# Optimization experiments

Measured on AMD Instinct MI355X. Metric: run time of the kernel, lower is better.

## Reference

```python
import jax, jax.numpy as jnp
import numpy as np

D_MODEL = 1024
D_STATE = 16
EXPANSION = 2
GROUPS = 16
D_INNER = EXPANSION * D_MODEL          # 2048
GROUP_SIZE = D_INNER // GROUPS         # 128
B, T = 2, 1024


def _rmsnorm(x, g, eps=1e-6):
    return x * jax.lax.rsqrt(jnp.mean(x * x, axis=-1, keepdims=True) + eps) * g


def setup_inputs() -> dict:
    key = jax.random.key(0)
    ks = jax.random.split(key, 8)
    s_in = 1.0 / np.sqrt(D_MODEL)
    s_inner = 1.0 / np.sqrt(D_INNER)
    s_ff = 1.0 / np.sqrt(4 * D_MODEL)
    return {
        "x": jax.random.normal(ks[0], (B, T, D_MODEL), dtype=jnp.float32),
        "A_log": jnp.log(jnp.linspace(1.0, float(D_STATE), D_STATE)).astype(jnp.float32),
        "g1": jnp.ones((D_MODEL,), jnp.float32),
        "g2": jnp.ones((D_MODEL,), jnp.float32),
        "W_in": jax.random.normal(ks[1], (2 * D_INNER, D_MODEL), jnp.float32) * s_in,
        "W_param": jax.random.normal(ks[2], (GROUPS * (1 + 2 * D_STATE), D_INNER), jnp.float32) * s_inner,
        "W_out": jax.random.normal(ks[3], (D_MODEL, D_INNER), jnp.float32) * s_inner,
        "W_ffn1": jax.random.normal(ks[4], (4 * D_MODEL, D_MODEL), jnp.float32) * s_in,
        "b_ffn1": jnp.zeros((4 * D_MODEL,), jnp.float32),
        "W_ffn2": jax.random.normal(ks[5], (D_MODEL, 4 * D_MODEL), jnp.float32) * s_ff,
        "b_ffn2": jnp.zeros((D_MODEL,), jnp.float32),
    }


def _ssm(u, delta, b, c, A_log):
    # u,delta: [B,T,D]; b,c: [B,T,D,N]. Sequential recurrence equivalent to
    # the module's chunked cumprod/cumsum formulation.
    A = -jnp.exp(A_log)                                   # [N]
    deltaA = jnp.clip(delta[..., None] * A, -10.0, 10.0)  # [B,T,D,N]
    expA = jnp.exp(deltaA)
    frac_exact = (expA - 1.0) / (A + 1e-12)
    frac = jnp.where(jnp.abs(deltaA) < 1e-4, delta[..., None], frac_exact)
    Bu = frac * (b * u[..., None])                        # [B,T,D,N]

    def step(h, inp):
        Ah_t, Bu_t, c_t = inp                             # [B,D,N] each
        h = Ah_t * h + Bu_t
        return h, jnp.sum(h * c_t, axis=-1)               # y_t: [B,D]

    tm = lambda a: jnp.moveaxis(a, 1, 0)                  # time-major [T,B,D,N]
    h0 = jnp.zeros(u.shape[:1] + u.shape[2:] + (A.shape[0],), u.dtype)
    _, ys = jax.lax.scan(step, h0, (tm(expA), tm(Bu), tm(c)))
    return jnp.moveaxis(ys, 0, 1)                         # [B,T,D]


def reference(x, A_log, g1, g2, W_in, W_param, W_out, W_ffn1, b_ffn1, W_ffn2, b_ffn2):
    Bsz, Tlen, _ = x.shape
    z = _rmsnorm(x, g1)
    xz_gate = jnp.einsum('btd,ed->bte', z, W_in)          # [B,T,2*D_inner]
    xz, gate = jnp.split(xz_gate, 2, axis=-1)
    xz = jax.nn.silu(xz)

    params = jnp.einsum('btd,pd->btp', xz, W_param)
    params = params.reshape(Bsz, Tlen, GROUPS, 1 + 2 * D_STATE)
    delta_g = params[..., :1]                             # [B,T,G,1]
    b_g = params[..., 1:1 + D_STATE]                      # [B,T,G,N]
    c_g = params[..., 1 + D_STATE:]                       # [B,T,G,N]
    delta = jax.nn.softplus(jnp.repeat(delta_g[..., 0], GROUP_SIZE, axis=2))  # [B,T,D_inner]
    b = jnp.repeat(b_g, GROUP_SIZE, axis=2)               # [B,T,D_inner,N]
    c = jnp.repeat(c_g, GROUP_SIZE, axis=2)

    y_ssm = _ssm(xz, delta, b, c, A_log)                  # [B,T,D_inner]
    y = y_ssm * jax.nn.silu(gate)
    y = jnp.einsum('bte,de->btd', y, W_out)
    x = x + y                                             # residual (dropout/droppath = identity in eval)

    h2 = _rmsnorm(x, g2)
    ffn = jnp.einsum('btf,df->btd',
                     jax.nn.silu(jnp.einsum('btd,fd->btf', h2, W_ffn1) + b_ffn1),
                     W_ffn2) + b_ffn2
    return x + ffn
```

## Files before the change

### kernel.cpp

```cpp
#include <hip/hip_runtime.h>
#include <hip/hip_bf16.h>
#include <stdint.h>

#define ROWS 2048
#define DM   1024
#define DI   2048
#define PPAD 640

typedef __bf16 bf16_t;
typedef __attribute__((ext_vector_type(8))) __bf16 bf16x8;
typedef __attribute__((ext_vector_type(4))) __bf16 bf16x4;
typedef __attribute__((ext_vector_type(4))) float f32x4;
typedef __attribute__((address_space(1))) void gvoid_t;
typedef __attribute__((address_space(3))) void lvoid_t;

__global__ __launch_bounds__(256) void prep0(const float* __restrict__ W_in,
                                             const float* __restrict__ W_param,
                                             bf16_t* o_in, bf16_t* o_par,
                                             const float* __restrict__ x,
                                             const float* __restrict__ g1,
                                             bf16_t* __restrict__ zb) {
  int tid = threadIdx.x;
  if (blockIdx.x >= 5376) {
    int row = blockIdx.x - 5376;
    const float4 v = *(const float4*)(x + (int64_t)row * DM + tid * 4);
    float ss = v.x * v.x + v.y * v.y + v.z * v.z + v.w * v.w;
#pragma unroll
    for (int o = 32; o; o >>= 1) ss += __shfl_xor(ss, o, 64);
    __shared__ float red[4];
    if ((tid & 63) == 0) red[tid >> 6] = ss;
    __syncthreads();
    float tot = red[0] + red[1] + red[2] + red[3];
    float sc = rsqrtf(tot * (1.0f / DM) + 1e-6f);
    const float4 gv = *(const float4*)(g1 + tid * 4);
    bf16_t* o = zb + (int64_t)row * DM + tid * 4;
    o[0] = (bf16_t)(v.x * sc * gv.x);
    o[1] = (bf16_t)(v.y * sc * gv.y);
    o[2] = (bf16_t)(v.z * sc * gv.z);
    o[3] = (bf16_t)(v.w * sc * gv.w);
    return;
  }
  if (blockIdx.x >= 4096) {
    int64_t e = (((int64_t)(blockIdx.x - 4096)) * 256 + tid) * 4;
    int row = (int)(e >> 11), col = (int)(e & 2047);
    float4 v = make_float4(0.f, 0.f, 0.f, 0.f);
    if (row < 528) v = *(const float4*)(W_param + (int64_t)row * 2048 + col);
    bf16_t* o = o_par + e;
    o[0] = (bf16_t)v.x; o[1] = (bf16_t)v.y; o[2] = (bf16_t)v.z; o[3] = (bf16_t)v.w;
    return;
  }
  int64_t e = ((int64_t)blockIdx.x * 256 + tid) * 4;
  float4 v = *(const float4*)(W_in + e);
  bf16_t* o = o_in + e;
  o[0] = (bf16_t)v.x; o[1] = (bf16_t)v.y; o[2] = (bf16_t)v.z; o[3] = (bf16_t)v.w;
}

__device__ __forceinline__ void conv3(int64_t c, int tid,
                                      const float* __restrict__ W_out,
                                      const float* __restrict__ W_f1,
                                      const float* __restrict__ W_f2,
                                      bf16_t* o_out, bf16_t* o_f1, bf16_t* o_f2) {
  const float* src; bf16_t* dst; int64_t e;
  if (c < 2048) { e = (c * 256 + tid) * 4; src = W_out; dst = o_out; }
  else if (c < 6144) { e = ((c - 2048) * 256 + tid) * 4; src = W_f1; dst = o_f1; }
  else { e = ((c - 6144) * 256 + tid) * 4; src = W_f2; dst = o_f2; }
  float4 v = *(const float4*)(src + e);
  bf16_t* o = dst + e;
  o[0] = (bf16_t)v.x; o[1] = (bf16_t)v.y; o[2] = (bf16_t)v.z; o[3] = (bf16_t)v.w;
}

__global__ __launch_bounds__(256) void cvt3_k(const float* __restrict__ W_out,
                                              const float* __restrict__ W_f1,
                                              const float* __restrict__ W_f2,
                                              bf16_t* o_out, bf16_t* o_f1,
                                              bf16_t* o_f2) {
  conv3(blockIdx.x, threadIdx.x, W_out, W_f1, W_f2, o_out, o_f1, o_f2);
}

__global__ __launch_bounds__(256) void rmsnorm_k(const float* __restrict__ x,
                                                 const float* __restrict__ g,
                                                 bf16_t* __restrict__ out) {
  int row = blockIdx.x;
  int tid = threadIdx.x;
  const float4 v = *(const float4*)(x + (int64_t)row * DM + tid * 4);
  float ss = v.x * v.x + v.y * v.y + v.z * v.z + v.w * v.w;
#pragma unroll
  for (int o = 32; o; o >>= 1) ss += __shfl_xor(ss, o, 64);
  __shared__ float red[4];
  if ((tid & 63) == 0) red[tid >> 6] = ss;
  __syncthreads();
  float tot = red[0] + red[1] + red[2] + red[3];
  float sc = rsqrtf(tot * (1.0f / DM) + 1e-6f);
  const float4 gv = *(const float4*)(g + tid * 4);
  bf16_t* o = out + (int64_t)row * DM + tid * 4;
  o[0] = (bf16_t)(v.x * sc * gv.x);
  o[1] = (bf16_t)(v.y * sc * gv.y);
  o[2] = (bf16_t)(v.z * sc * gv.z);
  o[3] = (bf16_t)(v.w * sc * gv.w);
}

__global__ __launch_bounds__(256) void silu_cvt(const float* __restrict__ in,
                                                bf16_t* __restrict__ out,
                                                int in_stride, int ncols) {
  int64_t e = ((int64_t)blockIdx.x * 256 + threadIdx.x) * 4;
  int row = (int)(e / ncols);
  int col = (int)(e % ncols);
  const float4 v = *(const float4*)(in + (int64_t)row * in_stride + col);
  bf16_t* o = out + e;
  o[0] = (bf16_t)(v.x / (1.f + expf(-v.x)));
  o[1] = (bf16_t)(v.y / (1.f + expf(-v.y)));
  o[2] = (bf16_t)(v.z / (1.f + expf(-v.z)));
  o[3] = (bf16_t)(v.w / (1.f + expf(-v.w)));
}

__global__ __launch_bounds__(256) void ssm_prep(const float* __restrict__ params,
                                                const float* __restrict__ A_log,
                                                float* __restrict__ ssmp) {
  int gid = blockIdx.x * 256 + threadIdx.x;
  int bg = gid >> 10, t = gid & 1023;
  int b = bg >> 4, g = bg & 15;
  const float* pr = params + (int64_t)(b * 1024 + t) * PPAD + g * 33;
  float raw = pr[0];
  float delta = raw > 0.f ? raw + log1pf(expf(-raw)) : log1pf(expf(raw));
  float* o = ssmp + (int64_t)gid * 48;
#pragma unroll
  for (int s = 0; s < 16; ++s) {
    float A = -expf(A_log[s]);
    float dA = delta * A;
    dA = fminf(10.f, fmaxf(-10.f, dA));
    float e = expf(dA);
    float frac = (fabsf(dA) < 1e-4f) ? delta : (e - 1.f) / (A + 1e-12f);
    o[s] = dA;
    o[16 + s] = frac * pr[1 + s];
    o[32 + s] = pr[17 + s];
  }
}

__global__ __launch_bounds__(256) void reduce_rms(const bf16_t* __restrict__ P,
                                                  const float* __restrict__ x,
                                                  const float* __restrict__ g,
                                                  float* __restrict__ xmid,
                                                  bf16_t* __restrict__ zb) {
  int row = blockIdx.x;
  int tid = threadIdx.x;
  int64_t base = (int64_t)row * DM + tid * 4;
  float4 v = *(const float4*)(x + base);
#pragma unroll
  for (int p = 0; p < 4; ++p) {
    bf16x4 pv = *(const bf16x4*)(P + (int64_t)p * ROWS * DM + base);
    v.x += (float)pv[0]; v.y += (float)pv[1]; v.z += (float)pv[2]; v.w += (float)pv[3];
  }
  *(float4*)(xmid + base) = v;
  float ss = v.x * v.x + v.y * v.y + v.z * v.z + v.w * v.w;
#pragma unroll
  for (int o = 32; o; o >>= 1) ss += __shfl_xor(ss, o, 64);
  __shared__ float red[4];
  if ((tid & 63) == 0) red[tid >> 6] = ss;
  __syncthreads();
  float tot = red[0] + red[1] + red[2] + red[3];
  float sc = rsqrtf(tot * (1.0f / DM) + 1e-6f);
  const float4 gv = *(const float4*)(g + tid * 4);
  bf16_t* o = zb + base;
  o[0] = (bf16_t)(v.x * sc * gv.x);
  o[1] = (bf16_t)(v.y * sc * gv.y);
  o[2] = (bf16_t)(v.z * sc * gv.z);
  o[3] = (bf16_t)(v.w * sc * gv.w);
}

__global__ __launch_bounds__(256) void reduce_bias(const bf16_t* __restrict__ P,
                                                   const float* __restrict__ res,
                                                   const float* __restrict__ bias,
                                                   float* __restrict__ out) {
  int64_t e = ((int64_t)blockIdx.x * 256 + threadIdx.x) * 4;
  int col = (int)(e % DM);
  float4 v = *(const float4*)(res + e);
  const float4 bv = *(const float4*)(bias + col);
  v.x += bv.x; v.y += bv.y; v.z += bv.z; v.w += bv.w;
#pragma unroll
  for (int p = 0; p < 4; ++p) {
    bf16x4 pv = *(const bf16x4*)(P + (int64_t)p * ROWS * DM + e);
    v.x += (float)pv[0]; v.y += (float)pv[1]; v.z += (float)pv[2]; v.w += (float)pv[3];
  }
  *(float4*)(out + e) = v;
}

__device__ __forceinline__ void prep_rows(const bf16_t* __restrict__ pb,
                                          const float* __restrict__ A_log,
                                          float* cf, int b, int g, int t0,
                                          int tid) {
  if (tid >= 64) return;
  int t = tid;
  int64_t row = (int64_t)(b * 1024) + t0 + t;
  float acc[33];
#pragma unroll
  for (int i = 0; i < 33; ++i) acc[i] = 0.f;
#pragma unroll
  for (int p = 0; p < 4; ++p) {
    const bf16_t* pr = pb + (int64_t)p * ROWS * PPAD + row * PPAD + g * 33;
#pragma unroll
    for (int i = 0; i < 33; ++i) acc[i] += (float)pr[i];
  }
  float raw = acc[0];
  float delta = raw > 0.f ? raw + log1pf(expf(-raw)) : log1pf(expf(raw));
  float* o = cf + t * 48;
#pragma unroll
  for (int s = 0; s < 16; ++s) {
    float A = -expf(A_log[s]);
    float dA = delta * A;
    dA = fminf(10.f, fmaxf(-10.f, dA));
    float e = expf(dA);
    float frac = (fabsf(dA) < 1e-4f) ? delta : (e - 1.f) / (A + 1e-12f);
    o[s] = dA;
    o[16 + s] = frac * acc[1 + s];
    o[32 + s] = acc[17 + s];
  }
}


template <int PREP>
__global__ __launch_bounds__(256) void ssm_chunk(const float* __restrict__ ssmp,
                                                 const bf16_t* __restrict__ pb,
                                                 const float* __restrict__ A_log,
                                                 const bf16_t* __restrict__ u,
                                                 float* __restrict__ S,
                                                 float* __restrict__ Etot) {
  __shared__ __align__(16) float cf[64 * 48];
  __shared__ __align__(16) float Lb[64 * 16];
  __shared__ __align__(16) bf16_t wl[16 * 64];
  __shared__ __align__(16) bf16_t Ut[128 * 64];
  int bgc = blockIdx.x;
  int bg = bgc >> 4, c = bgc & 15;
  int b = bg >> 4, g = bg & 15;
  int t0 = c * 64;
  int tid = threadIdx.x;
  {
    int lt = tid >> 4;
    int c8 = (tid & 15) * 8;
#pragma unroll
    for (int p = 0; p < 4; ++p) {
      int t = p * 16 + lt;
      bf16x8 v = *(const bf16x8*)(u + ((int64_t)(b * 1024) + t0 + t) * 2048 + g * 128 + c8);
#pragma unroll
      for (int j = 0; j < 8; ++j)
        Ut[(c8 + j) * 64 + (((t >> 3) ^ j) << 3) + (t & 7)] = v[j];
    }
  }
  if (PREP) {
    prep_rows(pb, A_log, cf, b, g, t0, tid);
  } else {
    const float4* src = (const float4*)(ssmp + ((int64_t)bg * 1024 + t0) * 48);
    float4* dst = (float4*)cf;
#pragma unroll
    for (int i = 0; i < 3; ++i) dst[i * 256 + tid] = src[i * 256 + tid];
  }
  __syncthreads();
  if (tid < 16) {
    float l = 0.f;
    for (int t = 0; t < 64; ++t) { l += cf[t * 48 + tid]; Lb[t * 16 + tid] = l; }
  }
  __syncthreads();
  {
    int s = tid >> 4, tb4 = (tid & 15) * 4;
    float lend = Lb[63 * 16 + s];
    bf16x4 wv;
#pragma unroll
    for (int j = 0; j < 4; ++j) {
      int t = tb4 + j;
      wv[j] = (bf16_t)(__expf(lend - Lb[t * 16 + s]) * cf[t * 48 + 16 + s]);
    }
    unsigned byo = (unsigned)(s * 128 + tb4 * 2) ^ ((unsigned)(s & 7) << 4);
    *(bf16x4*)((char*)wl + byo) = wv;
    if (tid < 16) Etot[(int64_t)bgc * 16 + tid] = __expf(Lb[63 * 16 + tid]);
  }
  __syncthreads();
  {
    int lane = tid & 63, wave = tid >> 6;
    int fr = lane & 15, kq = lane >> 4;
    f32x4 acc2[2] = {};
#pragma unroll
    for (int kk = 0; kk < 2; ++kk) {
      int kb = kk * 4 + kq;
      bf16x8 af = *(const bf16x8*)((const char*)wl +
                    ((unsigned)(fr * 128 + kb * 16) ^ ((unsigned)(fr & 7) << 4)));
#pragma unroll
      for (int q = 0; q < 2; ++q) {
        int ch = (wave * 2 + q) * 16 + fr;
        bf16x8 bfr = *(const bf16x8*)((const char*)Ut +
                       ((unsigned)(ch * 128 + kb * 16) ^ ((unsigned)(ch & 7) << 4)));
        acc2[q] = __builtin_amdgcn_mfma_f32_16x16x32_bf16(af, bfr, acc2[q], 0, 0, 0);
      }
    }
    float* Sp = S + (int64_t)bgc * 2048;
#pragma unroll
    for (int q = 0; q < 2; ++q) {
      int ch = (wave * 2 + q) * 16 + fr;
#pragma unroll
      for (int j = 0; j < 4; ++j) Sp[(kq * 4 + j) * 128 + ch] = acc2[q][j];
    }
  }
}

__global__ __launch_bounds__(256) void ssm_combine(const float* __restrict__ S,
                                                   const float* __restrict__ Etot,
                                                   float* __restrict__ H) {
  int gid = blockIdx.x * 256 + threadIdx.x;
  int bg = gid >> 11;
  int s = (gid >> 7) & 15;
  int ch = gid & 127;
  float h = 0.f;
  for (int c = 0; c < 16; ++c) {
    int bgc = bg * 16 + c;
    int64_t idx = ((int64_t)bgc * 16 + s) * 128 + ch;
    H[idx] = h;
    h = Etot[(int64_t)bgc * 16 + s] * h + S[idx];
  }
}

template <int PREP, int GM>
__global__ __launch_bounds__(256) void ssm_out(const float* __restrict__ ssmp,
                                               const bf16_t* __restrict__ pb,
                                               const float* __restrict__ A_log,
                                               const bf16_t* __restrict__ u,
                                               const float* __restrict__ H,
                                               const float* __restrict__ gate_f,
                                               const bf16_t* __restrict__ gate_b,
                                               int gstride,
                                               bf16_t* __restrict__ yout) {
  __shared__ __align__(16) float cf[64 * 48];
  __shared__ __align__(16) float Lb[64 * 16];
  __shared__ __align__(16) bf16_t Km[64 * 64];
  __shared__ __align__(16) bf16_t Ut[128 * 64];
  __shared__ __align__(16) bf16_t Hb[128 * 32];
  int bgc = blockIdx.x;
  int bg = bgc >> 4, c = bgc & 15;
  int b = bg >> 4, g = bg & 15;
  int t0 = c * 64;
  int tid = threadIdx.x;
  int lane = tid & 63, wave = tid >> 6;
  {
    int lt = tid >> 4;
    int c8 = (tid & 15) * 8;
#pragma unroll
    for (int p = 0; p < 4; ++p) {
      int t = p * 16 + lt;
      bf16x8 v = *(const bf16x8*)(u + ((int64_t)(b * 1024) + t0 + t) * 2048 + g * 128 + c8);
#pragma unroll
      for (int j = 0; j < 8; ++j)
        Ut[(c8 + j) * 64 + (((t >> 3) ^ j) << 3) + (t & 7)] = v[j];
    }
  }
  {
    int ch = tid >> 1, h8 = (tid & 1) * 8;
    const float* Hp = H + (int64_t)bgc * 2048 + ch;
#pragma unroll
    for (int j = 0; j < 8; ++j) {
      Hb[ch * 32 + h8 + j] = (bf16_t)Hp[(h8 + j) * 128];
      Hb[ch * 32 + 16 + h8 + j] = (bf16_t)0.f;
    }
  }
  if (PREP) {
    prep_rows(pb, A_log, cf, b, g, t0, tid);
  } else {
    const float4* src = (const float4*)(ssmp + ((int64_t)bg * 1024 + t0) * 48);
    float4* dst = (float4*)cf;
#pragma unroll
    for (int i = 0; i < 3; ++i) dst[i * 256 + tid] = src[i * 256 + tid];
  }
  __syncthreads();
  if (tid < 16) {
    float l = 0.f;
    for (int t = 0; t < 64; ++t) { l += cf[t * 48 + tid]; Lb[t * 16 + tid] = l; }
  }
  __syncthreads();
  {
    int t = tid >> 2, tp0 = (tid & 3) * 16;
    float4 cv[4], lv[4];
#pragma unroll
    for (int i = 0; i < 4; ++i) {
      cv[i] = *(const float4*)&cf[t * 48 + 32 + i * 4];
      lv[i] = *(const float4*)&Lb[t * 16 + i * 4];
    }
    float kv[16];
#pragma unroll
    for (int i = 0; i < 16; ++i) {
      int tp = tp0 + i;
      float k = 0.f;
      if (tp <= t) {
#pragma unroll
        for (int q = 0; q < 4; ++q) {
          float4 lpv = *(const float4*)&Lb[tp * 16 + q * 4];
          float4 fbv = *(const float4*)&cf[tp * 48 + 16 + q * 4];
          k += cv[q].x * __expf(lv[q].x - lpv.x) * fbv.x
             + cv[q].y * __expf(lv[q].y - lpv.y) * fbv.y
             + cv[q].z * __expf(lv[q].z - lpv.z) * fbv.z
             + cv[q].w * __expf(lv[q].w - lpv.w) * fbv.w;
        }
      }
      kv[i] = k;
    }
    bf16x8 lo, hi;
#pragma unroll
    for (int i = 0; i < 8; ++i) { lo[i] = (bf16_t)kv[i]; hi[i] = (bf16_t)kv[8 + i]; }
    unsigned b0 = (unsigned)(t * 128 + tp0 * 2) ^ ((unsigned)(t & 7) << 4);
    unsigned b1 = (unsigned)(t * 128 + tp0 * 2 + 16) ^ ((unsigned)(t & 7) << 4);
    *(bf16x8*)((char*)Km + b0) = lo;
    *(bf16x8*)((char*)Km + b1) = hi;
  }
  __syncthreads();
  int fr = lane & 15, kq = lane >> 4;
  int trow = (wave >> 1) * 32, wc = (wave & 1) * 64;
  f32x4 acc[2][4] = {};
#pragma unroll
  for (int kk = 0; kk < 2; ++kk) {
    int kb = kk * 4 + kq;
    bf16x8 af[2];
#pragma unroll
    for (int mi = 0; mi < 2; ++mi) {
      int row = trow + mi * 16 + fr;
      af[mi] = *(const bf16x8*)((const char*)Km +
                 ((unsigned)(row * 128 + kb * 16) ^ ((unsigned)(row & 7) << 4)));
    }
#pragma unroll
    for (int ni = 0; ni < 4; ++ni) {
      int ch = wc + ni * 16 + fr;
      bf16x8 bfr = *(const bf16x8*)((const char*)Ut +
                     ((unsigned)(ch * 128 + kb * 16) ^ ((unsigned)(ch & 7) << 4)));
#pragma unroll
      for (int mi = 0; mi < 2; ++mi)
        acc[mi][ni] = __builtin_amdgcn_mfma_f32_16x16x32_bf16(af[mi], bfr, acc[mi][ni], 0, 0, 0);
    }
  }
  {
    int s0 = kq * 8;
    bf16x8 cef[2];
    if (s0 < 16) {
#pragma unroll
      for (int mi = 0; mi < 2; ++mi) {
        int t = trow + mi * 16 + fr;
#pragma unroll
        for (int j = 0; j < 8; ++j)
          cef[mi][j] = (bf16_t)(cf[t * 48 + 32 + s0 + j] * __expf(Lb[t * 16 + s0 + j]));
      }
    } else {
#pragma unroll
      for (int mi = 0; mi < 2; ++mi)
#pragma unroll
        for (int j = 0; j < 8; ++j) cef[mi][j] = (bf16_t)0.f;
    }
#pragma unroll
    for (int ni = 0; ni < 4; ++ni) {
      int ch = wc + ni * 16 + fr;
      bf16x8 bhf = *(const bf16x8*)((const char*)Hb + ch * 64 + s0 * 2);
#pragma unroll
      for (int mi = 0; mi < 2; ++mi)
        acc[mi][ni] = __builtin_amdgcn_mfma_f32_16x16x32_bf16(cef[mi], bhf, acc[mi][ni], 0, 0, 0);
    }
  }
  {
    int64_t rowbase = (int64_t)b * 1024 + t0;
    int colbase = g * 128;
#pragma unroll
    for (int mi = 0; mi < 2; ++mi) {
#pragma unroll
      for (int ni = 0; ni < 4; ++ni) {
        int col = colbase + wc + ni * 16 + fr;
#pragma unroll
        for (int j = 0; j < 4; ++j) {
          int t = trow + mi * 16 + kq * 4 + j;
          float sg;
          if (GM) {
            sg = (float)gate_b[(rowbase + t) * 2048 + col];
          } else {
            float gv = gate_f[(rowbase + t) * (int64_t)gstride + col];
            sg = gv / (1.f + __expf(-gv));
          }
          yout[(rowbase + t) * 2048 + col] = (bf16_t)(acc[mi][ni][j] * sg);
        }
      }
    }
  }
}

template <int EPI>
__device__ __forceinline__ void epi_store(float v, int64_t r, int64_t cn, int N,
                                          float* Cz, const float* bias,
                                          const float* res, bf16_t* obf,
                                          bf16_t* ogate, int z) {
  if (EPI & 1) v += bias[cn];
  if (EPI & 2) v += res[r * N + cn];
  if (EPI & 4) {
    float sv = v / (1.f + __expf(-v));
    if (cn < 2048) obf[r * 2048 + cn] = (bf16_t)sv;
    else ogate[r * 2048 + cn - 2048] = (bf16_t)sv;
  } else if (EPI & 8) {
    obf[r * N + cn] = (bf16_t)(v / (1.f + __expf(-v)));
  } else if (EPI & 16) {
    obf[(int64_t)z * ROWS * N + r * N + cn] = (bf16_t)v;
  } else {
    Cz[r * N + cn] = v;
  }
}

__device__ __forceinline__ void xcd_swz(int& bx, int& by, int& bz) {
  int gx = gridDim.x, gy = gridDim.y, gz = gridDim.z;
  int flat = blockIdx.x + gx * (blockIdx.y + gy * blockIdx.z);
  int nwg = gx * gy * gz;
  int swz = flat;
  if ((nwg & 7) == 0) swz = (flat & 7) * (nwg >> 3) + (flat >> 3);
  bx = swz % gx;
  int rem = swz / gx;
  by = rem % gy;
  bz = rem / gy;
}

template <int EPI>
__global__ __launch_bounds__(256) void gemm_bt(const bf16_t* __restrict__ A,
                                               const bf16_t* __restrict__ Bw,
                                               float* __restrict__ C,
                                               const float* __restrict__ bias,
                                               const float* __restrict__ res,
                                               bf16_t* __restrict__ obf,
                                               bf16_t* __restrict__ ogate,
                                               int N, int Kps) {
  __shared__ bf16_t As[2][128 * 64];
  __shared__ bf16_t Bs[2][128 * 64];
  const int tid = threadIdx.x;
  const int wave = tid >> 6;
  const int lane = tid & 63;
  int bxi, byi, bzi;
  xcd_swz(bxi, byi, bzi);
  const int64_t m0 = (int64_t)byi * 128;
  const int64_t n0 = (int64_t)bxi * 128;
  const int K = Kps * gridDim.z;
  const int kbeg = bzi * Kps;
  float* Cz = C + (int64_t)bzi * ROWS * N;
  const int wm = (wave >> 1) * 64;
  const int wn = (wave & 1) * 64;
  f32x4 acc[4][4] = {};

  const int er = tid >> 3;
  const int ec = (tid * 8) & 63;
  const int fr = lane & 15;
  const int kq = (lane >> 4) * 8;

  auto stage = [&](int buf, int k0) {
#pragma unroll
    for (int i = 0; i < 4; ++i) {
      const bf16_t* ga = A + (m0 + er + i * 32) * K + k0 + ec;
      __builtin_amdgcn_global_load_lds((gvoid_t*)ga,
                                       (lvoid_t*)&As[buf][(i * 256 + wave * 64) * 8],
                                       16, 0, 0);
    }
#pragma unroll
    for (int i = 0; i < 4; ++i) {
      const bf16_t* gb = Bw + (n0 + er + i * 32) * K + k0 + ec;
      __builtin_amdgcn_global_load_lds((gvoid_t*)gb,
                                       (lvoid_t*)&Bs[buf][(i * 256 + wave * 64) * 8],
                                       16, 0, 0);
    }
  };
  auto compute = [&](int buf) {
#pragma unroll
    for (int kk = 0; kk < 2; ++kk) {
      bf16x8 af[4], bv[4];
#pragma unroll
      for (int mi = 0; mi < 4; ++mi)
        af[mi] = *reinterpret_cast<const bf16x8*>(&As[buf][(wm + mi * 16 + fr) * 64 + kk * 32 + kq]);
#pragma unroll
      for (int ni = 0; ni < 4; ++ni)
        bv[ni] = *reinterpret_cast<const bf16x8*>(&Bs[buf][(wn + ni * 16 + fr) * 64 + kk * 32 + kq]);
#pragma unroll
      for (int mi = 0; mi < 4; ++mi)
#pragma unroll
        for (int ni = 0; ni < 4; ++ni)
          acc[mi][ni] = __builtin_amdgcn_mfma_f32_16x16x32_bf16(af[mi], bv[ni], acc[mi][ni], 0, 0, 0);
    }
  };

  const int nk = Kps >> 6;
  stage(0, kbeg);
  asm volatile("s_waitcnt vmcnt(0)" ::: "memory");
  __builtin_amdgcn_s_barrier();
  int kc = kbeg;
  for (int t = 0; t < nk; t += 2) {
    stage(1, kc + 64);
    compute(0);
    asm volatile("s_waitcnt vmcnt(0)" ::: "memory");
    __builtin_amdgcn_s_barrier();
    if (t + 2 < nk) stage(0, kc + 128);
    compute(1);
    asm volatile("s_waitcnt vmcnt(0)" ::: "memory");
    __builtin_amdgcn_s_barrier();
    kc += 128;
  }

  const int crow = (lane >> 4) * 4;
  const int ccol = lane & 15;
#pragma unroll
  for (int mi = 0; mi < 4; ++mi)
#pragma unroll
    for (int ni = 0; ni < 4; ++ni)
#pragma unroll
      for (int j = 0; j < 4; ++j)
        epi_store<EPI>(acc[mi][ni][j], m0 + wm + mi * 16 + crow + j,
                       n0 + wn + ni * 16 + ccol, N, Cz, bias, res, obf, ogate,
                       bzi);
}

__global__ __launch_bounds__(256) void gemm_param_conv(
    const bf16_t* __restrict__ A, const bf16_t* __restrict__ Bw,
    bf16_t* __restrict__ pout,
    const float* __restrict__ W_out, const float* __restrict__ W_f1,
    const float* __restrict__ W_f2,
    bf16_t* o_out, bf16_t* o_f1, bf16_t* o_f2) {
  __shared__ bf16_t As[2][128 * 64];
  __shared__ bf16_t Bs[2][128 * 64];
  const int tid = threadIdx.x;
  if (blockIdx.x >= 320) {
    conv3(blockIdx.x - 320, tid, W_out, W_f1, W_f2, o_out, o_f1, o_f2);
    return;
  }
  const int flat = blockIdx.x;
  const int swz = (flat & 7) * 40 + (flat >> 3);
  const int bxi = swz % 5;
  const int byi = (swz / 5) % 16;
  const int bzi = swz / 80;
  const int wave = tid >> 6;
  const int lane = tid & 63;
  const int64_t m0 = (int64_t)byi * 128;
  const int64_t n0 = (int64_t)bxi * 128;
  const int K = 2048, Kps = 512;
  const int kbeg = bzi * Kps;
  const int wm = (wave >> 1) * 64;
  const int wn = (wave & 1) * 64;
  f32x4 acc[4][4] = {};
  const int er = tid >> 3;
  const int ec = (tid * 8) & 63;
  const int fr = lane & 15;
  const int kq = (lane >> 4) * 8;

  auto stage = [&](int buf, int k0) {
#pragma unroll
    for (int i = 0; i < 4; ++i) {
      const bf16_t* ga = A + (m0 + er + i * 32) * K + k0 + ec;
      __builtin_amdgcn_global_load_lds((gvoid_t*)ga,
                                       (lvoid_t*)&As[buf][(i * 256 + wave * 64) * 8],
                                       16, 0, 0);
    }
#pragma unroll
    for (int i = 0; i < 4; ++i) {
      const bf16_t* gb = Bw + (n0 + er + i * 32) * K + k0 + ec;
      __builtin_amdgcn_global_load_lds((gvoid_t*)gb,
                                       (lvoid_t*)&Bs[buf][(i * 256 + wave * 64) * 8],
                                       16, 0, 0);
    }
  };
  auto compute = [&](int buf) {
#pragma unroll
    for (int kk = 0; kk < 2; ++kk) {
      bf16x8 af[4], bv[4];
#pragma unroll
      for (int mi = 0; mi < 4; ++mi)
        af[mi] = *reinterpret_cast<const bf16x8*>(&As[buf][(wm + mi * 16 + fr) * 64 + kk * 32 + kq]);
#pragma unroll
      for (int ni = 0; ni < 4; ++ni)
        bv[ni] = *reinterpret_cast<const bf16x8*>(&Bs[buf][(wn + ni * 16 + fr) * 64 + kk * 32 + kq]);
#pragma unroll
      for (int mi = 0; mi < 4; ++mi)
#pragma unroll
        for (int ni = 0; ni < 4; ++ni)
          acc[mi][ni] = __builtin_amdgcn_mfma_f32_16x16x32_bf16(af[mi], bv[ni], acc[mi][ni], 0, 0, 0);
    }
  };

  const int nk = Kps >> 6;
  stage(0, kbeg);
  asm volatile("s_waitcnt vmcnt(0)" ::: "memory");
  __builtin_amdgcn_s_barrier();
  int kc = kbeg;
  for (int t = 0; t < nk; t += 2) {
    stage(1, kc + 64);
    compute(0);
    asm volatile("s_waitcnt vmcnt(0)" ::: "memory");
    __builtin_amdgcn_s_barrier();
    if (t + 2 < nk) stage(0, kc + 128);
    compute(1);
    asm volatile("s_waitcnt vmcnt(0)" ::: "memory");
    __builtin_amdgcn_s_barrier();
    kc += 128;
  }

  const int crow = (lane >> 4) * 4;
  const int ccol = lane & 15;
  bf16_t* pz = pout + (int64_t)bzi * ROWS * PPAD;
#pragma unroll
  for (int mi = 0; mi < 4; ++mi)
#pragma unroll
    for (int ni = 0; ni < 4; ++ni)
#pragma unroll
      for (int j = 0; j < 4; ++j) {
        int64_t r = m0 + wm + mi * 16 + crow + j;
        int64_t cn = n0 + wn + ni * 16 + ccol;
        pz[r * PPAD + cn] = (bf16_t)acc[mi][ni][j];
      }
}

template <int EPI>
__global__ __launch_bounds__(512, 2) void gemm_big(const bf16_t* __restrict__ A,
                                                   const bf16_t* __restrict__ Bw,
                                                   float* __restrict__ C,
                                                   const float* __restrict__ bias,
                                                   const float* __restrict__ res,
                                                   bf16_t* __restrict__ obf,
                                                   bf16_t* __restrict__ ogate,
                                                   int N, int Kps) {
  __shared__ bf16_t As[2][128 * 64];
  __shared__ bf16_t Bs[2][256 * 64];
  const int tid = threadIdx.x;
  const int wave = tid >> 6;
  const int lane = tid & 63;
  int bxi, byi, bzi;
  xcd_swz(bxi, byi, bzi);
  const int64_t m0 = (int64_t)byi * 128;
  const int64_t n0 = (int64_t)bxi * 256;
  const int K = Kps * gridDim.z;
  const int kbeg = bzi * Kps;
  float* Cz = C + (int64_t)bzi * ROWS * N;
  const int wm = (wave >> 2) * 64;
  const int wc = (wave & 3) * 64;
  const int fr = lane & 15;
  const int kq16 = (lane >> 4) * 16;
  const int er = tid >> 3;
  const int ec_sw = ((tid & 7) * 8) ^ ((er & 7) << 3);
  f32x4 acc[4][4] = {};

  auto stage = [&](int buf, int k0) {
#pragma unroll
    for (int i = 0; i < 2; ++i) {
      const bf16_t* ga = A + (m0 + er + i * 64) * K + k0 + ec_sw;
      __builtin_amdgcn_global_load_lds((gvoid_t*)ga,
          (lvoid_t*)((char*)&As[buf][0] + i * 8192 + wave * 1024), 16, 0, 0);
    }
#pragma unroll
    for (int i = 0; i < 4; ++i) {
      const bf16_t* gb = Bw + (n0 + er + i * 64) * K + k0 + ec_sw;
      __builtin_amdgcn_global_load_lds((gvoid_t*)gb,
          (lvoid_t*)((char*)&Bs[buf][0] + i * 8192 + wave * 1024), 16, 0, 0);
    }
  };

  const int nk = Kps >> 6;
  stage(0, kbeg);
  if (nk > 1) {
    stage(1, kbeg + 64);
    asm volatile("s_waitcnt vmcnt(6)" ::: "memory");
  } else {
    asm volatile("s_waitcnt vmcnt(0)" ::: "memory");
  }
  __builtin_amdgcn_s_barrier();
  __builtin_amdgcn_sched_barrier(0);

  for (int t = 0; t < nk; ++t) {
    const int buf = t & 1;
    bf16x8 af[2][4], bf[2][4];
#pragma unroll
    for (int kk = 0; kk < 2; ++kk) {
#pragma unroll
      for (int mi = 0; mi < 4; ++mi) {
        int r = wm + mi * 16 + fr;
        af[kk][mi] = *(const bf16x8*)((const char*)&As[buf][0] + r * 128 +
                       ((kk * 64 + kq16) ^ ((r & 7) << 4)));
      }
#pragma unroll
      for (int ni = 0; ni < 4; ++ni) {
        int r = wc + ni * 16 + fr;
        bf[kk][ni] = *(const bf16x8*)((const char*)&Bs[buf][0] + r * 128 +
                       ((kk * 64 + kq16) ^ ((r & 7) << 4)));
      }
    }
    asm volatile("s_waitcnt lgkmcnt(8)" ::: "memory");
    __builtin_amdgcn_sched_barrier(0);
    __builtin_amdgcn_s_setprio(1);
#pragma unroll
    for (int mi = 0; mi < 4; ++mi)
#pragma unroll
      for (int ni = 0; ni < 4; ++ni)
        acc[mi][ni] = __builtin_amdgcn_mfma_f32_16x16x32_bf16(
            af[0][mi], bf[0][ni], acc[mi][ni], 0, 0, 0);
    __builtin_amdgcn_s_setprio(0);
    __builtin_amdgcn_sched_barrier(0);
    asm volatile("s_waitcnt lgkmcnt(0)" ::: "memory");
    __builtin_amdgcn_sched_barrier(0);
    __builtin_amdgcn_s_barrier();
    __builtin_amdgcn_sched_barrier(0);
    if (t + 2 < nk) stage(buf, kbeg + (t + 2) * 64);
    __builtin_amdgcn_s_setprio(1);
#pragma unroll
    for (int mi = 0; mi < 4; ++mi)
#pragma unroll
      for (int ni = 0; ni < 4; ++ni)
        acc[mi][ni] = __builtin_amdgcn_mfma_f32_16x16x32_bf16(
            af[1][mi], bf[1][ni], acc[mi][ni], 0, 0, 0);
    __builtin_amdgcn_s_setprio(0);
    if (t + 1 < nk) {
      if (t + 2 < nk) asm volatile("s_waitcnt vmcnt(6)" ::: "memory");
      else            asm volatile("s_waitcnt vmcnt(0)" ::: "memory");
      __builtin_amdgcn_s_barrier();
      __builtin_amdgcn_sched_barrier(0);
    }
  }

  const int crow = (lane >> 4) * 4;
  const int ccol = lane & 15;
#pragma unroll
  for (int mi = 0; mi < 4; ++mi)
#pragma unroll
    for (int ni = 0; ni < 4; ++ni)
#pragma unroll
      for (int j = 0; j < 4; ++j)
        epi_store<EPI>(acc[mi][ni][j], m0 + wm + mi * 16 + crow + j,
                       n0 + wc + ni * 16 + ccol, N, Cz, bias, res, obf, ogate,
                       bzi);
}

extern "C" void kernel_launch(void* const* d_in, const int* in_sizes, int n_in,
                              void* d_out, int out_size, void* d_ws, size_t ws_size,
                              hipStream_t stream) {
  const float* x       = (const float*)d_in[0];
  const float* A_log   = (const float*)d_in[1];
  const float* g1      = (const float*)d_in[2];
  const float* g2      = (const float*)d_in[3];
  const float* W_in    = (const float*)d_in[4];
  const float* W_param = (const float*)d_in[5];
  const float* W_out   = (const float*)d_in[6];
  const float* W_ffn1  = (const float*)d_in[7];
  const float* b_ffn1  = (const float*)d_in[8];
  const float* W_ffn2  = (const float*)d_in[9];
  const float* b_ffn2  = (const float*)d_in[10];
  float* out = (float*)d_out;

  char* ws = (char*)d_ws;
  size_t off = 0;
  auto alloc = [&](size_t bytes) {
    char* p = ws + off;
    off += (bytes + 255) & ~(size_t)255;
    return p;
  };
  bf16_t* wb_in  = (bf16_t*)alloc(4096ull * 1024 * 2);
  bf16_t* wb_par = (bf16_t*)alloc((size_t)PPAD * 2048 * 2);
  bf16_t* wb_out = (bf16_t*)alloc(1024ull * 2048 * 2);
  bf16_t* wb_f1  = (bf16_t*)alloc(4096ull * 1024 * 2);
  bf16_t* wb_f2  = (bf16_t*)alloc(1024ull * 4096 * 2);
  bf16_t* zbuf   = (bf16_t*)alloc(2048ull * 1024 * 2);
  float*  xzg    = (float*)alloc(2048ull * 4096 * 4);
  float*  params = (float*)alloc(2048ull * PPAD * 4);
  float*  ssmp   = (float*)alloc(32ull * 1024 * 48 * 4);
  float*  xmid   = (float*)alloc(2048ull * 1024 * 4);
  char*   regA   = alloc(2048ull * 4096 * 2);
  bf16_t* xz_act = (bf16_t*)regA;
  bf16_t* y_b16  = (bf16_t*)(regA + 2048ull * 2048 * 2);
  bf16_t* f_act  = (bf16_t*)regA;
  bf16_t* sgate  = (bf16_t*)xzg;
  float* Sbuf = params;
  float* Etot = params + 32ull * 16 * 16 * 128;
  float* Hbuf = xmid;
  float*  psum = (float*)alloc(4ull * ROWS * 1024 * 4);
  bf16_t* pb16 = (bf16_t*)psum;
  const bool sk = (off <= ws_size);

  dim3 b256(256), b512(512);
  prep0<<<7424, b256, 0, stream>>>(W_in, W_param, wb_in, wb_par, x, g1, zbuf);

  if (sk) {
    gemm_big<4><<<dim3(16, 16), b512, 0, stream>>>(zbuf, wb_in, psum, nullptr, nullptr, xz_act, sgate, 4096, 1024);
    gemm_param_conv<<<10560, b256, 0, stream>>>(xz_act, wb_par, pb16,
                                                W_out, W_ffn1, W_ffn2,
                                                wb_out, wb_f1, wb_f2);
    ssm_chunk<1><<<512, b256, 0, stream>>>(nullptr, pb16, A_log, xz_act, Sbuf, Etot);
    ssm_combine<<<256, b256, 0, stream>>>(Sbuf, Etot, Hbuf);
    ssm_out<1, 1><<<512, b256, 0, stream>>>(nullptr, pb16, A_log, xz_act, Hbuf, nullptr, sgate, 2048, y_b16);
    gemm_big<16><<<dim3(4, 16, 4), b512, 0, stream>>>(y_b16, wb_out, psum, nullptr, nullptr, pb16, nullptr, 1024, 512);
    reduce_rms<<<2048, b256, 0, stream>>>(pb16, x, g2, xmid, zbuf);
    gemm_big<9><<<dim3(16, 16), b512, 0, stream>>>(zbuf, wb_f1, psum, b_ffn1, nullptr, f_act, nullptr, 4096, 1024);
    gemm_big<16><<<dim3(4, 16, 4), b512, 0, stream>>>(f_act, wb_f2, psum, nullptr, nullptr, pb16, nullptr, 1024, 1024);
    reduce_bias<<<2048, b256, 0, stream>>>(pb16, xmid, b_ffn2, out);
  } else {
    cvt3_k<<<10240, b256, 0, stream>>>(W_out, W_ffn1, W_ffn2, wb_out, wb_f1, wb_f2);
    gemm_bt<0><<<dim3(32, 16), b256, 0, stream>>>(zbuf, wb_in, xzg, nullptr, nullptr, nullptr, nullptr, 4096, 1024);
    silu_cvt<<<4096, b256, 0, stream>>>(xzg, xz_act, 4096, 2048);
    gemm_bt<0><<<dim3(PPAD / 128, 16), b256, 0, stream>>>(xz_act, wb_par, params, nullptr, nullptr, nullptr, nullptr, PPAD, 2048);
    ssm_prep<<<128, b256, 0, stream>>>(params, A_log, ssmp);
    ssm_chunk<0><<<512, b256, 0, stream>>>(ssmp, nullptr, A_log, xz_act, Sbuf, Etot);
    ssm_combine<<<256, b256, 0, stream>>>(Sbuf, Etot, Hbuf);
    ssm_out<0, 0><<<512, b256, 0, stream>>>(ssmp, nullptr, A_log, xz_act, Hbuf, xzg + 2048, nullptr, 4096, y_b16);
    gemm_bt<2><<<dim3(8, 16), b256, 0, stream>>>(y_b16, wb_out, xmid, nullptr, x, nullptr, nullptr, 1024, 2048);
    rmsnorm_k<<<2048, b256, 0, stream>>>(xmid, g2, zbuf);
    gemm_bt<1><<<dim3(32, 16), b256, 0, stream>>>(zbuf, wb_f1, xzg, b_ffn1, nullptr, nullptr, nullptr, 4096, 1024);
    silu_cvt<<<8192, b256, 0, stream>>>(xzg, f_act, 4096, 4096);
    gemm_bt<3><<<dim3(8, 16), b256, 0, stream>>>(f_act, wb_f2, out, b_ffn2, xmid, nullptr, nullptr, 1024, 4096);
  }
}
```

Before: 176.8 us.

## Fuse chunk-state combine into ssm_out and triple-buffer gemm_big LDS

Removes the ssm_combine kernel: each ssm_out block now recomputes its incoming chunk state by scanning the preceding chunk summaries (S, Etot) directly, trading a launch and an H round-trip for redundant serial work in later chunks. Separately, gemm_big moves to three LDS buffers with a prefetch distance of two. This drops the per-iteration lgkmcnt wait and barrier before staging, and the occupancy hint of two blocks per CU is removed. The larger LDS footprint may cut occupancy, and the remaining sync must still keep the buffer reuse race-free.

```diff
diff --git a/kernel.cpp b/kernel.cpp
--- a/kernel.cpp
+++ b/kernel.cpp
@@ -300,28 +300,13 @@
   }
 }
 
-__global__ __launch_bounds__(256) void ssm_combine(const float* __restrict__ S,
-                                                   const float* __restrict__ Etot,
-                                                   float* __restrict__ H) {
-  int gid = blockIdx.x * 256 + threadIdx.x;
-  int bg = gid >> 11;
-  int s = (gid >> 7) & 15;
-  int ch = gid & 127;
-  float h = 0.f;
-  for (int c = 0; c < 16; ++c) {
-    int bgc = bg * 16 + c;
-    int64_t idx = ((int64_t)bgc * 16 + s) * 128 + ch;
-    H[idx] = h;
-    h = Etot[(int64_t)bgc * 16 + s] * h + S[idx];
-  }
-}
-
 template <int PREP, int GM>
 __global__ __launch_bounds__(256) void ssm_out(const float* __restrict__ ssmp,
                                                const bf16_t* __restrict__ pb,
                                                const float* __restrict__ A_log,
                                                const bf16_t* __restrict__ u,
-                                               const float* __restrict__ H,
+                                               const float* __restrict__ S,
+                                               const float* __restrict__ Etot,
                                                const float* __restrict__ gate_f,
                                                const bf16_t* __restrict__ gate_b,
                                                int gstride,
@@ -350,12 +335,22 @@
     }
   }
   {
-    int ch = tid >> 1, h8 = (tid & 1) * 8;
-    const float* Hp = H + (int64_t)bgc * 2048 + ch;
+    int ch = tid & 127, s0 = (tid >> 7) * 8;
+    const float* Sp = S + (int64_t)(bg * 16) * 2048;
+    const float* Ep = Etot + (int64_t)(bg * 16) * 16;
+    float h[8];
+#pragma unroll
+    for (int j = 0; j < 8; ++j) h[j] = 0.f;
+    for (int cc = 0; cc < c; ++cc) {
+#pragma unroll
+      for (int j = 0; j < 8; ++j)
+        h[j] = Ep[cc * 16 + s0 + j] * h[j] +
+               Sp[(int64_t)cc * 2048 + (s0 + j) * 128 + ch];
+    }
 #pragma unroll
     for (int j = 0; j < 8; ++j) {
-      Hb[ch * 32 + h8 + j] = (bf16_t)Hp[(h8 + j) * 128];
-      Hb[ch * 32 + 16 + h8 + j] = (bf16_t)0.f;
+      Hb[ch * 32 + s0 + j] = (bf16_t)h[j];
+      Hb[ch * 32 + 16 + s0 + j] = (bf16_t)0.f;
     }
   }
   if (PREP) {
@@ -706,16 +701,16 @@
 }
 
 template <int EPI>
-__global__ __launch_bounds__(512, 2) void gemm_big(const bf16_t* __restrict__ A,
-                                                   const bf16_t* __restrict__ Bw,
-                                                   float* __restrict__ C,
-                                                   const float* __restrict__ bias,
-                                                   const float* __restrict__ res,
-                                                   bf16_t* __restrict__ obf,
-                                                   bf16_t* __restrict__ ogate,
-                                                   int N, int Kps) {
-  __shared__ bf16_t As[2][128 * 64];
-  __shared__ bf16_t Bs[2][256 * 64];
+__global__ __launch_bounds__(512) void gemm_big(const bf16_t* __restrict__ A,
+                                                const bf16_t* __restrict__ Bw,
+                                                float* __restrict__ C,
+                                                const float* __restrict__ bias,
+                                                const float* __restrict__ res,
+                                                bf16_t* __restrict__ obf,
+                                                bf16_t* __restrict__ ogate,
+                                                int N, int Kps) {
+  __shared__ bf16_t As[3][128 * 64];
+  __shared__ bf16_t Bs[3][256 * 64];
   const int tid = threadIdx.x;
   const int wave = tid >> 6;
   const int lane = tid & 63;
@@ -761,7 +756,7 @@
   __builtin_amdgcn_sched_barrier(0);
 
   for (int t = 0; t < nk; ++t) {
-    const int buf = t & 1;
+    const int buf = t % 3;
     bf16x8 af[2][4], bf[2][4];
 #pragma unroll
     for (int kk = 0; kk < 2; ++kk) {
@@ -789,11 +784,7 @@
             af[0][mi], bf[0][ni], acc[mi][ni], 0, 0, 0);
     __builtin_amdgcn_s_setprio(0);
     __builtin_amdgcn_sched_barrier(0);
-    asm volatile("s_waitcnt lgkmcnt(0)" ::: "memory");
-    __builtin_amdgcn_sched_barrier(0);
-    __builtin_amdgcn_s_barrier();
-    __builtin_amdgcn_sched_barrier(0);
-    if (t + 2 < nk) stage(buf, kbeg + (t + 2) * 64);
+    if (t + 2 < nk) stage((t + 2) % 3, kbeg + (t + 2) * 64);
     __builtin_amdgcn_s_setprio(1);
 #pragma unroll
     for (int mi = 0; mi < 4; ++mi)
@@ -863,7 +854,6 @@
   bf16_t* sgate  = (bf16_t*)xzg;
   float* Sbuf = params;
   float* Etot = params + 32ull * 16 * 16 * 128;
-  float* Hbuf = xmid;
   float*  psum = (float*)alloc(4ull * ROWS * 1024 * 4);
   bf16_t* pb16 = (bf16_t*)psum;
   const bool sk = (off <= ws_size);
@@ -877,8 +867,7 @@
                                                 W_out, W_ffn1, W_ffn2,
                                                 wb_out, wb_f1, wb_f2);
     ssm_chunk<1><<<512, b256, 0, stream>>>(nullptr, pb16, A_log, xz_act, Sbuf, Etot);
-    ssm_combine<<<256, b256, 0, stream>>>(Sbuf, Etot, Hbuf);
-    ssm_out<1, 1><<<512, b256, 0, stream>>>(nullptr, pb16, A_log, xz_act, Hbuf, nullptr, sgate, 2048, y_b16);
+    ssm_out<1, 1><<<512, b256, 0, stream>>>(nullptr, pb16, A_log, xz_act, Sbuf, Etot, nullptr, sgate, 2048, y_b16);
     gemm_big<16><<<dim3(4, 16, 4), b512, 0, stream>>>(y_b16, wb_out, psum, nullptr, nullptr, pb16, nullptr, 1024, 512);
     reduce_rms<<<2048, b256, 0, stream>>>(pb16, x, g2, xmid, zbuf);
     gemm_big<9><<<dim3(16, 16), b512, 0, stream>>>(zbuf, wb_f1, psum, b_ffn1, nullptr, f_act, nullptr, 4096, 1024);
@@ -891,8 +880,7 @@
     gemm_bt<0><<<dim3(PPAD / 128, 16), b256, 0, stream>>>(xz_act, wb_par, params, nullptr, nullptr, nullptr, nullptr, PPAD, 2048);
     ssm_prep<<<128, b256, 0, stream>>>(params, A_log, ssmp);
     ssm_chunk<0><<<512, b256, 0, stream>>>(ssmp, nullptr, A_log, xz_act, Sbuf, Etot);
-    ssm_combine<<<256, b256, 0, stream>>>(Sbuf, Etot, Hbuf);
-    ssm_out<0, 0><<<512, b256, 0, stream>>>(ssmp, nullptr, A_log, xz_act, Hbuf, xzg + 2048, nullptr, 4096, y_b16);
+    ssm_out<0, 0><<<512, b256, 0, stream>>>(ssmp, nullptr, A_log, xz_act, Sbuf, Etot, xzg + 2048, nullptr, 4096, y_b16);
     gemm_bt<2><<<dim3(8, 16), b256, 0, stream>>>(y_b16, wb_out, xmid, nullptr, x, nullptr, nullptr, 1024, 2048);
     rmsnorm_k<<<2048, b256, 0, stream>>>(xmid, g2, zbuf);
     gemm_bt<1><<<dim3(32, 16), b256, 0, stream>>>(zbuf, wb_f1, xzg, b_ffn1, nullptr, nullptr, nullptr, 4096, 1024);
```

Measured after the change: 170.7 us. 1.04x faster.
